# Kernel tuning notes

Measured on AMD Instinct MI355X. Metric: run time of the kernel, lower is better.

## Reference

```python
import jax, jax.numpy as jnp
import numpy as np

HEADS, DIM_HEAD, LANDMARKS, PINV_ITERS, CONV_K = 8, 64, 256, 6, 33


def iter_pinv(x, iters=PINV_ITERS):
    # Moore-Penrose iterative pseudo-inverse (lucidrains nystrom_attention)
    abs_x = jnp.abs(x)
    scale = abs_x.sum(-1).max() * abs_x.sum(-2).max()  # global maxes, as in torch.max
    z = jnp.swapaxes(x, -1, -2) / scale
    I = jnp.eye(x.shape[-1], dtype=x.dtype)
    for _ in range(iters):
        xz = x @ z
        z = 0.25 * z @ (13.0 * I - xz @ (15.0 * I - xz @ (7.0 * I - xz)))
    return z


def nystrom_attention(h, W_qkv, W_out, b_out, conv_w):
    b, n, _ = h.shape
    inner = HEADS * DIM_HEAD
    qkv = h @ W_qkv  # (b, n, 3*inner), bias=False
    q, k, v = jnp.split(qkv, 3, axis=-1)
    split_heads = lambda t: t.reshape(b, n, HEADS, DIM_HEAD).transpose(0, 2, 1, 3)
    q, k, v = split_heads(q), split_heads(k), split_heads(v)  # (b,h,n,dh)
    q = q * (DIM_HEAD ** -0.5)
    l = n // LANDMARKS  # tokens per landmark (n divisible by m, so no padding)
    q_l = q.reshape(b, HEADS, LANDMARKS, l, DIM_HEAD).mean(3)
    k_l = k.reshape(b, HEADS, LANDMARKS, l, DIM_HEAD).mean(3)
    sim1 = jnp.einsum('bhnd,bhmd->bhnm', q, k_l)      # (b,h,n,m)
    sim2 = jnp.einsum('bhmd,bhld->bhml', q_l, k_l)    # (b,h,m,m)
    sim3 = jnp.einsum('bhmd,bhnd->bhmn', q_l, k)      # (b,h,m,n)
    attn1 = jax.nn.softmax(sim1, -1)
    attn2 = jax.nn.softmax(sim2, -1)
    attn3 = jax.nn.softmax(sim3, -1)
    out = (attn1 @ iter_pinv(attn2)) @ (attn3 @ v)    # (b,h,n,dh)
    # residual depthwise conv along sequence dim: Conv2d(heads, heads, (33,1), groups=heads, no bias)
    res = jax.lax.conv_general_dilated(
        v, conv_w, window_strides=(1, 1),
        padding=((CONV_K // 2, CONV_K // 2), (0, 0)),
        feature_group_count=HEADS)
    out = out + res
    out = out.transpose(0, 2, 1, 3).reshape(b, n, inner)
    return out @ W_out + b_out


def setup_inputs() -> dict:
    key = jax.random.key(0)
    ks = jax.random.split(key, 8)
    N, Din, Dout = 8192, 1024, 256
    inner = HEADS * DIM_HEAD
    s = 0.02
    return {
        'x': jax.random.normal(ks[0], (1, N, Din), jnp.float32),
        'W_ft': jax.random.normal(ks[1], (Din, Dout), jnp.float32) * s,
        'b_ft': jnp.zeros((Dout,), jnp.float32),
        'W_qkv': jax.random.normal(ks[2], (Dout, 3 * inner), jnp.float32) * s,
        'W_out': jax.random.normal(ks[3], (inner, Dout), jnp.float32) * s,
        'b_out': jnp.zeros((Dout,), jnp.float32),
        'conv_w': jax.random.normal(ks[4], (HEADS, 1, CONV_K, 1), jnp.float32) * s,
        'W_score': jax.random.normal(ks[5], (Dout, 1), jnp.float32) * s,
        'b_score': jnp.zeros((1,), jnp.float32),
    }


def reference(x, W_ft, b_ft, W_qkv, W_out, b_out, conv_w, W_score, b_score):
    # feature_transform: Linear -> Dropout (identity in eval) -> ReLU
    h = jax.nn.relu(x @ W_ft + b_ft)                 # (1, N, Dout)
    af = nystrom_attention(h, W_qkv, W_out, b_out, conv_w)
    # score_layer: Linear -> Dropout -> ReLU
    scores = jax.nn.relu(af @ W_score + b_score)     # (1, N, 1)
    scores = scores[0].T                             # (1, N)
    weights = jax.nn.softmax(scores, axis=1)         # (1, N)
    aggregated = weights @ h[0]                      # (1, Dout)
    return aggregated, weights
```

## Files before the change

### kernel.cpp

```cpp
#include <hip/hip_runtime.h>

typedef unsigned short u16;
typedef __attribute__((ext_vector_type(8))) short s16x8;
typedef __attribute__((ext_vector_type(4))) float f32x4;
typedef __attribute__((ext_vector_type(8))) unsigned short u16x8;

__device__ inline float b2f(u16 u) {
  unsigned x = ((unsigned)u) << 16;
  return __builtin_bit_cast(float, x);
}
__device__ inline u16 f2b(float f) {
  unsigned u = __builtin_bit_cast(unsigned, f);
  u += 0x7fffu + ((u >> 16) & 1u);
  return (u16)(u >> 16);
}

#define GLL(src, dst) __builtin_amdgcn_global_load_lds( \
    (const __attribute__((address_space(1))) unsigned int*)(src), \
    (__attribute__((address_space(3))) unsigned int*)(dst), 16, 0, 0)

struct MP {
  const u16* A; const u16* B;
  u16* C; u16* Ct; float* Cf; u16* vTo;
  const u16* Aadd; const float* bias;
  int M, N, K;
  int lda, ldb, ldc, ldct, ldcf, ldaadd;
  long long bA, bB, bC, bCt, bCf, bAadd;
  float alpha, beta;
  int relu, scale_cols; float colscale;
  int kchunks;
};

template<int BM, int BN, bool F32A>
__global__ __launch_bounds__(256) void gemm_mfma(MP p)
{
  constexpr int WM = BM / 2, WN = BN / 2;
  constexpr int FM = WM / 16, FN = WN / 16;
  constexpr int APAN = BM / 16, BPAN = BN / 16, NPAN = APAN + BPAN;
  constexpr int APW = (APAN + 3) / 4;
  __shared__ __align__(16) u16 lds[2 * NPAN * 512];

  const int tid = threadIdx.x, lane = tid & 63, wid = tid >> 6;
  const int bz = blockIdx.z;
  const int batch = (p.kchunks > 1) ? bz / p.kchunks : bz;
  const int kc    = (p.kchunks > 1) ? bz % p.kchunks : 0;
  const u16* A = p.A + (long long)batch * p.bA + (long long)kc * p.K;
  const float* Af32 = (const float*)p.A + (long long)batch * p.bA + (long long)kc * p.K;
  const u16* B = p.B + (long long)batch * p.bB + (long long)kc * p.K;
  const int m0 = blockIdx.y * BM, n0 = blockIdx.x * BN;
  const int srow = lane & 15, skoff = (lane >> 4) * 8;
  const int wm0 = (wid >> 1) * WM, wn0 = (wid & 1) * WN;

  f32x4 acc[FM][FN];
#pragma unroll
  for (int i = 0; i < FM; i++)
#pragma unroll
    for (int j = 0; j < FN; j++) acc[i][j] = (f32x4){0.f, 0.f, 0.f, 0.f};

  float4 areg[APW][2];

  auto stage_all = [&](int sb, int kt) {
#pragma unroll
    for (int pp = wid; pp < NPAN; pp += 4) {
      const u16* src = (pp < APAN)
        ? A + (size_t)(m0 + pp * 16 + srow) * p.lda + kt + skoff
        : B + (size_t)(n0 + (pp - APAN) * 16 + srow) * p.ldb + kt + skoff;
      GLL(src, &lds[sb * (NPAN * 512) + pp * 512]);
    }
  };
  auto stage_b = [&](int sb, int kt) {
#pragma unroll
    for (int pp = APAN + wid; pp < NPAN; pp += 4) {
      const u16* src = B + (size_t)(n0 + (pp - APAN) * 16 + srow) * p.ldb + kt + skoff;
      GLL(src, &lds[sb * (NPAN * 512) + pp * 512]);
    }
  };
  auto load_a = [&](int kt) {
#pragma unroll
    for (int ap = 0; ap < APW; ap++) {
      int pp = wid + ap * 4;
      const float* src = Af32 + (size_t)(m0 + pp * 16 + srow) * p.lda + kt + skoff;
      areg[ap][0] = ((const float4*)src)[0];
      areg[ap][1] = ((const float4*)src)[1];
    }
  };
  auto write_a = [&](int sb) {
#pragma unroll
    for (int ap = 0; ap < APW; ap++) {
      int pp = wid + ap * 4;
      u16 t[8];
      t[0] = f2b(areg[ap][0].x); t[1] = f2b(areg[ap][0].y);
      t[2] = f2b(areg[ap][0].z); t[3] = f2b(areg[ap][0].w);
      t[4] = f2b(areg[ap][1].x); t[5] = f2b(areg[ap][1].y);
      t[6] = f2b(areg[ap][1].z); t[7] = f2b(areg[ap][1].w);
      *(s16x8*)&lds[sb * (NPAN * 512) + pp * 512 + lane * 8] = *(const s16x8*)t;
    }
  };
  auto compute = [&](int sb) {
    const int bo = sb * (NPAN * 512);
    s16x8 afr[FM], bfr[FN];
#pragma unroll
    for (int i = 0; i < FM; i++)
      afr[i] = *(const s16x8*)&lds[bo + (wm0 / 16 + i) * 512 + lane * 8];
#pragma unroll
    for (int j = 0; j < FN; j++)
      bfr[j] = *(const s16x8*)&lds[bo + (APAN + wn0 / 16 + j) * 512 + lane * 8];
#pragma unroll
    for (int i = 0; i < FM; i++)
#pragma unroll
      for (int j = 0; j < FN; j++)
        acc[i][j] = __builtin_amdgcn_mfma_f32_16x16x32_bf16(afr[i], bfr[j], acc[i][j], 0, 0, 0);
  };

  const int nt = p.K / 32;
  int buf = 0;
  if constexpr (F32A) { load_a(0); stage_b(0, 0); write_a(0); }
  else                { stage_all(0, 0); }
  asm volatile("s_waitcnt vmcnt(0)" ::: "memory");
  __syncthreads();

  for (int t = 0; t < nt; ++t) {
    if constexpr (F32A) {
      if (t + 1 < nt) { load_a((t + 1) * 32); stage_b(buf ^ 1, (t + 1) * 32); }
      compute(buf);
      if (t + 1 < nt) write_a(buf ^ 1);
    } else {
      if (t + 1 < nt) stage_all(buf ^ 1, (t + 1) * 32);
      compute(buf);
    }
    asm volatile("s_waitcnt vmcnt(0)" ::: "memory");
    __syncthreads();
    buf ^= 1;
  }

  const int r0 = (lane >> 4) * 4, c0 = lane & 15;
#pragma unroll
  for (int i = 0; i < FM; i++) {
#pragma unroll
    for (int j = 0; j < FN; j++) {
#pragma unroll
      for (int q = 0; q < 4; q++) {
        const int gr = m0 + wm0 + i * 16 + r0 + q;
        const int gc = n0 + wn0 + j * 16 + c0;
        float c = p.alpha * acc[i][j][q];
        if (p.Aadd) c += p.beta * b2f(p.Aadd[(long long)batch * p.bAadd + (size_t)gr * p.ldaadd + gc]);
        if (p.bias) c += p.bias[gc];
        if (gc < p.scale_cols) c *= p.colscale;
        if (p.relu) c = fmaxf(c, 0.f);
        if (p.Cf) p.Cf[(long long)bz * p.bCf + (size_t)gr * p.ldcf + gc] = c;
        u16 b = f2b(c);
        if (p.C)  p.C [(long long)batch * p.bC + (size_t)gr * p.ldc + gc] = b;
        if (p.Ct) p.Ct[(long long)batch * p.bCt + (size_t)gc * p.ldct + gr] = b;
        if (p.vTo && gc >= 1024) p.vTo[(size_t)(gc - 1024) * 8192 + gr] = b;
      }
    }
  }
}

struct AVF { const u16 *qkvb, *ql, *vT; float *Cf, *den; };

__global__ __launch_bounds__(256) void av_fused(AVF p)
{
  __shared__ __align__(16) u16 lds[20480];
  const int tid = threadIdx.x, lane = tid & 63, wid = tid >> 6;
  const int bz = blockIdx.z, head = bz >> 4, kc = bz & 15;
  const int m0 = blockIdx.y * 128;
  const int srow = lane & 15, skoff = (lane >> 4) * 8;
  const int r0 = (lane >> 4) * 4, c0 = lane & 15;
  const u16* Kb = p.qkvb + 512 + (size_t)(kc * 512) * 1536 + head * 64;
  const u16* Vb = p.vT + (size_t)head * 524288 + kc * 512;
  const u16* QL = p.ql + head * 16384 + (size_t)m0 * 64;

#pragma unroll
  for (int q = 0; q < 4; q++) {
    int pid = wid * 4 + q, pr = pid >> 1, kc2 = pid & 1;
    GLL(QL + (size_t)(pr * 16 + srow) * 64 + kc2 * 32 + skoff, &lds[pid * 512]);
  }
  auto stage_kv = [&](int sb, int t) {
    int kr = wid >> 1, kc2 = wid & 1;
    GLL(Kb + (size_t)(t * 32 + kr * 16 + srow) * 1536 + kc2 * 32 + skoff,
        &lds[8192 + sb * 2048 + wid * 512]);
    GLL(Vb + (size_t)(wid * 16 + srow) * 8192 + t * 32 + skoff,
        &lds[12288 + sb * 2048 + wid * 512]);
  };

  f32x4 acc[4][2];
#pragma unroll
  for (int i = 0; i < 4; i++)
#pragma unroll
    for (int j = 0; j < 2; j++) acc[i][j] = (f32x4){0.f, 0.f, 0.f, 0.f};
  float den[2][4];
#pragma unroll
  for (int i = 0; i < 2; i++)
#pragma unroll
    for (int q = 0; q < 4; q++) den[i][q] = 0.f;

  const int nt = 16;
  int buf = 0;
  stage_kv(0, 0);
  asm volatile("s_waitcnt vmcnt(0)" ::: "memory");
  __syncthreads();

  for (int t = 0; t < nt; ++t) {
    if (t + 1 < nt) stage_kv(buf ^ 1, t + 1);
    f32x4 s[2][2];
#pragma unroll
    for (int i = 0; i < 2; i++)
#pragma unroll
      for (int j = 0; j < 2; j++) s[i][j] = (f32x4){0.f, 0.f, 0.f, 0.f};
#pragma unroll
    for (int t2 = 0; t2 < 2; t2++) {
      s16x8 aq[2], bk[2];
#pragma unroll
      for (int i = 0; i < 2; i++)
        aq[i] = *(const s16x8*)&lds[((wid * 2 + i) * 2 + t2) * 512 + lane * 8];
#pragma unroll
      for (int j = 0; j < 2; j++)
        bk[j] = *(const s16x8*)&lds[8192 + buf * 2048 + (j * 2 + t2) * 512 + lane * 8];
#pragma unroll
      for (int i = 0; i < 2; i++)
#pragma unroll
        for (int j = 0; j < 2; j++)
          s[i][j] = __builtin_amdgcn_mfma_f32_16x16x32_bf16(aq[i], bk[j], s[i][j], 0, 0, 0);
    }
#pragma unroll
    for (int i = 0; i < 2; i++)
#pragma unroll
      for (int j = 0; j < 2; j++)
#pragma unroll
        for (int q = 0; q < 4; q++) {
          float e = expf(s[i][j][q]);
          den[i][q] += e;
          int kk = j * 16 + c0;
          lds[16384 + (wid * 2 + i) * 512 + (r0 + q) * 8 + (kk >> 3) * 128 + (kk & 7)] = f2b(e);
        }
    asm volatile("s_waitcnt vmcnt(0)" ::: "memory");
    __syncthreads();
    {
      s16x8 afr[4], bfr[2];
#pragma unroll
      for (int i = 0; i < 4; i++)
        afr[i] = *(const s16x8*)&lds[16384 + ((wid >> 1) * 4 + i) * 512 + lane * 8];
#pragma unroll
      for (int j = 0; j < 2; j++)
        bfr[j] = *(const s16x8*)&lds[12288 + buf * 2048 + ((wid & 1) * 2 + j) * 512 + lane * 8];
#pragma unroll
      for (int i = 0; i < 4; i++)
#pragma unroll
        for (int j = 0; j < 2; j++)
          acc[i][j] = __builtin_amdgcn_mfma_f32_16x16x32_bf16(afr[i], bfr[j], acc[i][j], 0, 0, 0);
    }
    __syncthreads();
    buf ^= 1;
  }

#pragma unroll
  for (int i = 0; i < 4; i++)
#pragma unroll
    for (int j = 0; j < 2; j++)
#pragma unroll
      for (int q = 0; q < 4; q++) {
        const int gr = m0 + (wid >> 1) * 64 + i * 16 + r0 + q;
        const int gc = (wid & 1) * 32 + j * 16 + c0;
        p.Cf[(size_t)bz * 16384 + (size_t)gr * 64 + gc] = acc[i][j][q];
      }
#pragma unroll
  for (int i = 0; i < 2; i++)
#pragma unroll
    for (int q = 0; q < 4; q++) {
      float v = den[i][q];
      v += __shfl_xor(v, 1); v += __shfl_xor(v, 2);
      v += __shfl_xor(v, 4); v += __shfl_xor(v, 8);
      if (c0 == 0)
        p.den[(size_t)bz * 256 + m0 + wid * 32 + i * 16 + r0 + q] = v;
    }
}

struct FA1 { const u16 *qkvb, *kl, *MmT; u16 *af; };

__global__ __launch_bounds__(256) void fused_attn1(FA1 p)
{
  __shared__ __align__(16) u16 lds[36864];
  __shared__ float mb[4][64];
  const int tid = threadIdx.x, lane = tid & 63, wid = tid >> 6;
  const int head = blockIdx.y, n0 = blockIdx.x * 64;
  const int srow = lane & 15, skoff = (lane >> 4) * 8;
  const int rbase = (lane >> 4) * 4;

  for (int pid = wid; pid < 72; pid += 4) {
    const u16* src;
    if (pid < 8) {
      int pr = pid >> 1, kc = pid & 1;
      src = p.qkvb + (size_t)(n0 + pr * 16 + srow) * 1536 + head * 64 + kc * 32 + skoff;
    } else if (pid < 40) {
      int j = pid - 8, pr = j >> 1, kc = j & 1;
      src = p.kl + head * 16384 + (size_t)(pr * 16 + srow) * 64 + kc * 32 + skoff;
    } else {
      int j = pid - 40, pr = j >> 3, kc = j & 7;
      src = p.MmT + head * 16384 + (size_t)(pr * 16 + srow) * 256 + kc * 32 + skoff;
    }
    GLL(src, &lds[pid * 512]);
  }
  asm volatile("s_waitcnt vmcnt(0)" ::: "memory");
  __syncthreads();

  const int wr = (wid >> 1) * 32, ch_ = wid & 1;
  f32x4 s[2][8];
#pragma unroll
  for (int i = 0; i < 2; i++)
#pragma unroll
    for (int j = 0; j < 8; j++) s[i][j] = (f32x4){0.f, 0.f, 0.f, 0.f};
#pragma unroll
  for (int t = 0; t < 2; t++) {
    s16x8 a[2], b[8];
#pragma unroll
    for (int i = 0; i < 2; i++)
      a[i] = *(const s16x8*)&lds[(((wid >> 1) * 2 + i) * 2 + t) * 512 + lane * 8];
#pragma unroll
    for (int j = 0; j < 8; j++)
      b[j] = *(const s16x8*)&lds[4096 + ((ch_ * 8 + j) * 2 + t) * 512 + lane * 8];
#pragma unroll
    for (int i = 0; i < 2; i++)
#pragma unroll
      for (int j = 0; j < 8; j++)
        s[i][j] = __builtin_amdgcn_mfma_f32_16x16x32_bf16(a[i], b[j], s[i][j], 0, 0, 0);
  }
#pragma unroll
  for (int i = 0; i < 2; i++)
#pragma unroll
    for (int q = 0; q < 4; q++) {
      float rm = -INFINITY;
#pragma unroll
      for (int j = 0; j < 8; j++) rm = fmaxf(rm, s[i][j][q]);
#pragma unroll
      for (int off = 1; off < 16; off <<= 1) rm = fmaxf(rm, __shfl_xor(rm, off));
      if ((lane & 15) == 0) mb[ch_][wr + i * 16 + rbase + q] = rm;
    }
  __syncthreads();
  float m_[2][4];
#pragma unroll
  for (int i = 0; i < 2; i++)
#pragma unroll
    for (int q = 0; q < 4; q++)
      m_[i][q] = fmaxf(mb[0][wr + i * 16 + rbase + q], mb[1][wr + i * 16 + rbase + q]);
#pragma unroll
  for (int i = 0; i < 2; i++)
#pragma unroll
    for (int q = 0; q < 4; q++) {
      float ss = 0.f;
#pragma unroll
      for (int j = 0; j < 8; j++) {
        float e = expf(s[i][j][q] - m_[i][q]);
        s[i][j][q] = e; ss += e;
      }
#pragma unroll
      for (int off = 1; off < 16; off <<= 1) ss += __shfl_xor(ss, off);
      if ((lane & 15) == 0) mb[2 + ch_][wr + i * 16 + rbase + q] = ss;
    }
  __syncthreads();
#pragma unroll
  for (int i = 0; i < 2; i++)
#pragma unroll
    for (int q = 0; q < 4; q++) {
      int row = wr + i * 16 + rbase + q;
      float inv = 1.f / (mb[2][row] + mb[3][row]);
#pragma unroll
      for (int j = 0; j < 8; j++)
        lds[(size_t)row * 264 + ch_ * 128 + j * 16 + (lane & 15)] = f2b(s[i][j][q] * inv);
    }
  __syncthreads();
  const int wr2 = (wid >> 1) * 32, wd2 = (wid & 1) * 32;
  f32x4 acc[2][2];
#pragma unroll
  for (int i = 0; i < 2; i++)
#pragma unroll
    for (int jd = 0; jd < 2; jd++) acc[i][jd] = (f32x4){0.f, 0.f, 0.f, 0.f};
#pragma unroll
  for (int t = 0; t < 8; t++) {
    s16x8 a[2], b[2];
#pragma unroll
    for (int i = 0; i < 2; i++)
      a[i] = *(const s16x8*)&lds[(size_t)(wr2 + i * 16 + (lane & 15)) * 264 + t * 32 + (lane >> 4) * 8];
#pragma unroll
    for (int jd = 0; jd < 2; jd++)
      b[jd] = *(const s16x8*)&lds[20480 + (((wid & 1) * 2 + jd) * 8 + t) * 512 + lane * 8];
#pragma unroll
    for (int i = 0; i < 2; i++)
#pragma unroll
      for (int jd = 0; jd < 2; jd++)
        acc[i][jd] = __builtin_amdgcn_mfma_f32_16x16x32_bf16(a[i], b[jd], acc[i][jd], 0, 0, 0);
  }
#pragma unroll
  for (int i = 0; i < 2; i++)
#pragma unroll
    for (int jd = 0; jd < 2; jd++)
#pragma unroll
      for (int q = 0; q < 4; q++)
        p.af[(size_t)(n0 + wr2 + i * 16 + rbase + q) * 512 + head * 64 + wd2 + jd * 16 + (lane & 15)]
            = f2b(acc[i][jd][q]);
}

__global__ void conv_res_add_bf16(const u16* __restrict__ qkvb,
                                  const float* __restrict__ convw,
                                  u16* __restrict__ af)
{
  __shared__ float vt[96][64];
  const int h = blockIdx.y, n0 = blockIdx.x * 64;
  const int t = threadIdx.x, ch = t & 63, r0 = t >> 6;
  for (int r = r0; r < 96; r += 4) {
    int n = n0 - 16 + r;
    float v = 0.f;
    if (n >= 0 && n < 8192) v = b2f(qkvb[(size_t)n * 1536 + 1024 + h * 64 + ch]);
    vt[r][ch] = v;
  }
  __syncthreads();
  float w[33];
#pragma unroll
  for (int j = 0; j < 33; j++) w[j] = convw[h * 33 + j];
  for (int tl = r0; tl < 64; tl += 4) {
    float acc = 0.f;
#pragma unroll
    for (int j = 0; j < 33; j++) acc += w[j] * vt[tl + j][ch];
    size_t o = (size_t)(n0 + tl) * 512 + h * 64 + ch;
    af[o] = f2b(b2f(af[o]) + acc);
  }
}

__global__ void reduce_bias_bf16(const float* __restrict__ parts, int nparts,
                                 const float* __restrict__ bias, int relu,
                                 u16* __restrict__ out,
                                 const float* __restrict__ Wscore,
                                 const float* __restrict__ bscore,
                                 float* __restrict__ scores)
{
  const int i4 = blockIdx.x * 256 + threadIdx.x;
  float4 s = ((const float4*)parts)[i4];
  for (int k = 1; k < nparts; k++) {
    float4 v = ((const float4*)parts)[(size_t)k * 524288 + i4];
    s.x += v.x; s.y += v.y; s.z += v.z; s.w += v.w;
  }
  const float4 b = ((const float4*)bias)[i4 & 63];
  s.x += b.x; s.y += b.y; s.z += b.z; s.w += b.w;
  if (relu) {
    s.x = fmaxf(s.x, 0.f); s.y = fmaxf(s.y, 0.f);
    s.z = fmaxf(s.z, 0.f); s.w = fmaxf(s.w, 0.f);
  }
  if (out) {
    ushort4 o; o.x = f2b(s.x); o.y = f2b(s.y); o.z = f2b(s.z); o.w = f2b(s.w);
    ((ushort4*)out)[i4] = o;
  }
  if (Wscore) {
    const int lane = threadIdx.x & 63;
    const float4 w = ((const float4*)Wscore)[lane];
    float v = s.x * w.x + s.y * w.y + s.z * w.z + s.w * w.w;
    for (int off = 32; off; off >>= 1) v += __shfl_down(v, off);
    if (lane == 0)
      scores[blockIdx.x * 4 + (threadIdx.x >> 6)] = fmaxf(v + bscore[0], 0.f);
  }
}

__global__ void fused_tail(const float* __restrict__ scores,
                           const u16* __restrict__ hb, float* __restrict__ out)
{
  __shared__ float red[256];
  const int t = threadIdx.x, c = blockIdx.x;
  float e[32];
  float m = -INFINITY;
#pragma unroll
  for (int i = 0; i < 32; i++) { e[i] = scores[t + i * 256]; m = fmaxf(m, e[i]); }
  red[t] = m; __syncthreads();
  for (int s = 128; s; s >>= 1) { if (t < s) red[t] = fmaxf(red[t], red[t + s]); __syncthreads(); }
  m = red[0]; __syncthreads();
  float ls = 0.f;
#pragma unroll
  for (int i = 0; i < 32; i++) { e[i] = expf(e[i] - m); ls += e[i]; }
  red[t] = ls; __syncthreads();
  for (int s = 128; s; s >>= 1) { if (t < s) red[t] += red[t + s]; __syncthreads(); }
  const float inv = 1.f / red[0];
  __syncthreads();

  if (c < 256) {
    float acc = 0.f;
#pragma unroll
    for (int i = 0; i < 32; i++)
      acc += e[i] * inv * b2f(hb[(size_t)(t + i * 256) * 256 + c]);
    red[t] = acc; __syncthreads();
    for (int s = 128; s; s >>= 1) { if (t < s) red[t] += red[t + s]; __syncthreads(); }
    if (t == 0) out[c] = red[0];
  } else {
#pragma unroll
    for (int i = 0; i < 32; i++) out[256 + t + i * 256] = e[i] * inv;
  }
}

__global__ void prescale(const u16* __restrict__ x2, float* __restrict__ sbuf)
{
  const int h = blockIdx.x, t = threadIdx.x;
  const u16* X = x2 + ((size_t)h << 16);
  float cs = 0.f;
  for (int r = 0; r < 256; r++) cs += fabsf(b2f(X[r * 256 + t]));
  float rs = 0.f;
  for (int c4 = 0; c4 < 256; c4 += 4) {
    ushort4 v = *(const ushort4*)(X + (size_t)t * 256 + c4);
    rs += fabsf(b2f(v.x)) + fabsf(b2f(v.y)) + fabsf(b2f(v.z)) + fabsf(b2f(v.w));
  }
  __shared__ float red[512];
  red[t] = rs; red[256 + t] = cs;
  __syncthreads();
  for (int s = 128; s; s >>= 1) {
    if (t < s) {
      red[t] = fmaxf(red[t], red[t + s]);
      red[256 + t] = fmaxf(red[256 + t], red[256 + t + s]);
    }
    __syncthreads();
  }
  if (t == 0) { sbuf[h] = red[0]; sbuf[8 + h] = red[256]; }
}

__global__ void pinv_init(const u16* __restrict__ x2, const float* __restrict__ sbuf,
                          u16* __restrict__ z0, u16* __restrict__ z0T)
{
  __shared__ u16 tile[64][80];
  const int t = threadIdx.x;
  const size_t base = (size_t)blockIdx.y << 16;
  const int tr = (blockIdx.x >> 2) * 64, tc = (blockIdx.x & 3) * 64;
  const u16* X = x2 + base;

  float mr = -INFINITY, mc = -INFINITY;
#pragma unroll
  for (int i = 0; i < 8; i++) {
    mr = fmaxf(mr, sbuf[i]);
    mc = fmaxf(mc, sbuf[8 + i]);
  }
  const float inv = 1.f / (mr * mc);

  {
    int r = t >> 2, cg = (t & 3) * 16;
#pragma unroll
    for (int v4 = 0; v4 < 4; v4++) {
      ushort4 v = *(const ushort4*)(X + (size_t)(tr + r) * 256 + tc + cg + v4 * 4);
      v.x = f2b(b2f(v.x) * inv); v.y = f2b(b2f(v.y) * inv);
      v.z = f2b(b2f(v.z) * inv); v.w = f2b(b2f(v.w) * inv);
      *(ushort4*)(z0T + base + (size_t)(tr + r) * 256 + tc + cg + v4 * 4) = v;
      *(ushort4*)&tile[r][cg + v4 * 4] = v;
    }
  }
  __syncthreads();
  {
    int c = t >> 2, rg = (t & 3) * 16;
    u16 o[16];
#pragma unroll
    for (int e = 0; e < 16; e++) o[e] = tile[rg + e][c];
#pragma unroll
    for (int v4 = 0; v4 < 4; v4++)
      *(ushort4*)(z0 + base + (size_t)(tc + c) * 256 + tr + rg + v4 * 4) = *(ushort4*)&o[v4 * 4];
  }
}

struct PG {
  const u16 *U, *V, *Xadd, *XaddT;
  u16 *DR, *DT;
  float alpha, beta;
};

template<bool WD, bool WDT>
__global__ __launch_bounds__(256) void pinv_gemm(PG p)
{
  __shared__ __align__(16) u16 lds[65536 / 2];
  const int tid = threadIdx.x, lane = tid & 63, wid = tid >> 6;
  const size_t base = (size_t)blockIdx.z << 16;
  const u16* U = p.U + base;
  const u16* V = p.V + base;
  const int m0 = blockIdx.y * 64, n0 = blockIdx.x * 64;
  const int srow = lane & 15, skoff = (lane >> 4) * 8;
  const int wr = (wid >> 1) * 32, wc = (wid & 1) * 32;

#pragma unroll
  for (int q = 0; q < 16; q++) {
    const int pid = wid * 16 + q;
    const int rg = (pid >> 3) & 3, t = pid & 7;
    const u16* src = (pid < 32)
      ? U + (size_t)(m0 + rg * 16 + srow) * 256 + t * 32 + skoff
      : V + (size_t)(n0 + rg * 16 + srow) * 256 + t * 32 + skoff;
    GLL(src, &lds[pid * 512]);
  }
  asm volatile("s_waitcnt vmcnt(0)" ::: "memory");
  __syncthreads();

  f32x4 acc[2][2], accT[2][2];
#pragma unroll
  for (int i = 0; i < 2; i++)
#pragma unroll
    for (int j = 0; j < 2; j++) {
      acc[i][j] = (f32x4){0.f, 0.f, 0.f, 0.f};
      accT[i][j] = (f32x4){0.f, 0.f, 0.f, 0.f};
    }

#pragma unroll
  for (int t = 0; t < 8; t++) {
    s16x8 afr[2], bfr[2];
#pragma unroll
    for (int i = 0; i < 2; i++)
      afr[i] = *(const s16x8*)&lds[((wr / 16 + i) * 8 + t) * 512 + lane * 8];
#pragma unroll
    for (int j = 0; j < 2; j++)
      bfr[j] = *(const s16x8*)&lds[(32 + (wc / 16 + j) * 8 + t) * 512 + lane * 8];
#pragma unroll
    for (int i = 0; i < 2; i++)
#pragma unroll
      for (int j = 0; j < 2; j++) {
        if constexpr (WD)
          acc[i][j] = __builtin_amdgcn_mfma_f32_16x16x32_bf16(afr[i], bfr[j], acc[i][j], 0, 0, 0);
        if constexpr (WDT)
          accT[j][i] = __builtin_amdgcn_mfma_f32_16x16x32_bf16(bfr[j], afr[i], accT[j][i], 0, 0, 0);
      }
  }

  const int r0 = (lane >> 4) * 4, c0 = lane & 15;
  if constexpr (WD) {
    const u16* Xa = p.Xadd ? p.Xadd + base : nullptr;
    u16* DR = p.DR + base;
#pragma unroll
    for (int i = 0; i < 2; i++)
#pragma unroll
      for (int j = 0; j < 2; j++)
#pragma unroll
        for (int q = 0; q < 4; q++) {
          const int gr = m0 + wr + i * 16 + r0 + q;
          const int gc = n0 + wc + j * 16 + c0;
          float v = p.alpha * acc[i][j][q];
          if (Xa) v += p.beta * b2f(Xa[(size_t)gr * 256 + gc]);
          DR[(size_t)gr * 256 + gc] = f2b(v);
        }
  }
  if constexpr (WDT) {
    const u16* Xt = p.XaddT ? p.XaddT + base : nullptr;
    u16* DT = p.DT + base;
#pragma unroll
    for (int j = 0; j < 2; j++)
#pragma unroll
      for (int i = 0; i < 2; i++)
#pragma unroll
        for (int q = 0; q < 4; q++) {
          const int gn = n0 + wc + j * 16 + r0 + q;
          const int gm = m0 + wr + i * 16 + c0;
          float v = p.alpha * accT[j][i][q];
          if (Xt) v += p.beta * b2f(Xt[(size_t)gn * 256 + gm]);
          DT[(size_t)gn * 256 + gm] = f2b(v);
        }
  }
}

struct PR1 { const u16 *A, *At, *z; u16 *B, *Bt, *G, *Gt, *W; };

__global__ __launch_bounds__(256) void pinv_r1(PR1 p)
{
  __shared__ __align__(16) u16 lds[32768];
  const int tid = threadIdx.x, lane = tid & 63, wid = tid >> 6;
  const int prob = blockIdx.z >> 3;
  const size_t base = (size_t)(blockIdx.z & 7) << 16;
  const u16* U = (prob ? p.z : p.A) + base;
  const u16* V = p.At + base;
  const int m0 = blockIdx.y * 64, n0 = blockIdx.x * 64;
  const int srow = lane & 15, skoff = (lane >> 4) * 8;
  const int wr = (wid >> 1) * 32, wc = (wid & 1) * 32;

#pragma unroll
  for (int q = 0; q < 16; q++) {
    const int pid = wid * 16 + q;
    const int rg = (pid >> 3) & 3, t = pid & 7;
    const u16* src = (pid < 32)
      ? U + (size_t)(m0 + rg * 16 + srow) * 256 + t * 32 + skoff
      : V + (size_t)(n0 + rg * 16 + srow) * 256 + t * 32 + skoff;
    GLL(src, &lds[pid * 512]);
  }
  asm volatile("s_waitcnt vmcnt(0)" ::: "memory");
  __syncthreads();

  f32x4 acc[2][2], accT[2][2];
#pragma unroll
  for (int i = 0; i < 2; i++)
#pragma unroll
    for (int j = 0; j < 2; j++) {
      acc[i][j] = (f32x4){0.f, 0.f, 0.f, 0.f};
      accT[i][j] = (f32x4){0.f, 0.f, 0.f, 0.f};
    }

#pragma unroll
  for (int t = 0; t < 8; t++) {
    s16x8 afr[2], bfr[2];
#pragma unroll
    for (int i = 0; i < 2; i++)
      afr[i] = *(const s16x8*)&lds[((wr / 16 + i) * 8 + t) * 512 + lane * 8];
#pragma unroll
    for (int j = 0; j < 2; j++)
      bfr[j] = *(const s16x8*)&lds[(32 + (wc / 16 + j) * 8 + t) * 512 + lane * 8];
#pragma unroll
    for (int i = 0; i < 2; i++)
#pragma unroll
      for (int j = 0; j < 2; j++) {
        acc[i][j] = __builtin_amdgcn_mfma_f32_16x16x32_bf16(afr[i], bfr[j], acc[i][j], 0, 0, 0);
        if (prob == 0)
          accT[j][i] = __builtin_amdgcn_mfma_f32_16x16x32_bf16(bfr[j], afr[i], accT[j][i], 0, 0, 0);
      }
  }

  const int r0 = (lane >> 4) * 4, c0 = lane & 15;
  if (prob == 0) {
    const u16* Ab  = p.A  + base;
    const u16* Atb = p.At + base;
    u16 *Bv = p.B + base, *Btv = p.Bt + base;
    u16 *Gv = p.G + base, *Gtv = p.Gt + base;
#pragma unroll
    for (int i = 0; i < 2; i++)
#pragma unroll
      for (int j = 0; j < 2; j++)
#pragma unroll
        for (int q = 0; q < 4; q++) {
          const int gr = m0 + wr + i * 16 + r0 + q;
          const int gc = n0 + wc + j * 16 + c0;
          float b = acc[i][j][q];
          float a = b2f(Ab[(size_t)gr * 256 + gc]);
          Bv[(size_t)gr * 256 + gc] = f2b(b);
          Gv[(size_t)gr * 256 + gc] = f2b(7.f * a - b);
        }
#pragma unroll
    for (int j = 0; j < 2; j++)
#pragma unroll
      for (int i = 0; i < 2; i++)
#pragma unroll
        for (int q = 0; q < 4; q++) {
          const int gn = n0 + wc + j * 16 + r0 + q;
          const int gm = m0 + wr + i * 16 + c0;
          float bt = accT[j][i][q];
          float at = b2f(Atb[(size_t)gn * 256 + gm]);
          Btv[(size_t)gn * 256 + gm] = f2b(bt);
          Gtv[(size_t)gn * 256 + gm] = f2b(7.f * at - bt);
        }
  } else {
    u16* Wv = p.W + base;
#pragma unroll
    for (int i = 0; i < 2; i++)
#pragma unroll
      for (int j = 0; j < 2; j++)
#pragma unroll
        for (int q = 0; q < 4; q++) {
          const int gr = m0 + wr + i * 16 + r0 + q;
          const int gc = n0 + wc + j * 16 + c0;
          Wv[(size_t)gr * 256 + gc] = f2b(acc[i][j][q]);
        }
  }
}

struct PR2 { const u16 *W, *G, *Gt, *B, *Bt, *z, *A, *At; u16 *zo, *Ao, *Aot; };

__global__ __launch_bounds__(256) void pinv_r2(PR2 p)
{
  __shared__ __align__(16) u16 lds[32768];
  const int tid = threadIdx.x, lane = tid & 63, wid = tid >> 6;
  const int prob = blockIdx.z >> 3;
  const size_t base = (size_t)(blockIdx.z & 7) << 16;
  const u16* U = (prob ? p.G  : p.W ) + base;
  const u16* V = (prob ? p.Bt : p.Gt) + base;
  const int m0 = blockIdx.y * 64, n0 = blockIdx.x * 64;
  const int srow = lane & 15, skoff = (lane >> 4) * 8;
  const int wr = (wid >> 1) * 32, wc = (wid & 1) * 32;

#pragma unroll
  for (int q = 0; q < 16; q++) {
    const int pid = wid * 16 + q;
    const int rg = (pid >> 3) & 3, t = pid & 7;
    const u16* src = (pid < 32)
      ? U + (size_t)(m0 + rg * 16 + srow) * 256 + t * 32 + skoff
      : V + (size_t)(n0 + rg * 16 + srow) * 256 + t * 32 + skoff;
    GLL(src, &lds[pid * 512]);
  }
  asm volatile("s_waitcnt vmcnt(0)" ::: "memory");
  __syncthreads();

  f32x4 acc[2][2], accT[2][2];
#pragma unroll
  for (int i = 0; i < 2; i++)
#pragma unroll
    for (int j = 0; j < 2; j++) {
      acc[i][j] = (f32x4){0.f, 0.f, 0.f, 0.f};
      accT[i][j] = (f32x4){0.f, 0.f, 0.f, 0.f};
    }

#pragma unroll
  for (int t = 0; t < 8; t++) {
    s16x8 afr[2], bfr[2];
#pragma unroll
    for (int i = 0; i < 2; i++)
      afr[i] = *(const s16x8*)&lds[((wr / 16 + i) * 8 + t) * 512 + lane * 8];
#pragma unroll
    for (int j = 0; j < 2; j++)
      bfr[j] = *(const s16x8*)&lds[(32 + (wc / 16 + j) * 8 + t) * 512 + lane * 8];
#pragma unroll
    for (int i = 0; i < 2; i++)
#pragma unroll
      for (int j = 0; j < 2; j++) {
        acc[i][j] = __builtin_amdgcn_mfma_f32_16x16x32_bf16(afr[i], bfr[j], acc[i][j], 0, 0, 0);
        if (prob)
          accT[j][i] = __builtin_amdgcn_mfma_f32_16x16x32_bf16(bfr[j], afr[i], accT[j][i], 0, 0, 0);
      }
  }

  const int r0 = (lane >> 4) * 4, c0 = lane & 15;
  if (prob == 0) {
    const u16* Zb = p.z + base;
    const u16* Wb = p.W + base;
    u16* Zo = p.zo + base;
#pragma unroll
    for (int i = 0; i < 2; i++)
#pragma unroll
      for (int j = 0; j < 2; j++)
#pragma unroll
        for (int q = 0; q < 4; q++) {
          const int gr = m0 + wr + i * 16 + r0 + q;
          const int gc = n0 + wc + j * 16 + c0;
          float v = 0.25f * acc[i][j][q]
                  + 3.25f * b2f(Zb[(size_t)gr * 256 + gc])
                  - 3.75f * b2f(Wb[(size_t)gr * 256 + gc]);
          Zo[(size_t)gr * 256 + gc] = f2b(v);
        }
  } else {
    const u16* Ab  = p.A  + base;
    const u16* Bb  = p.B  + base;
    const u16* Atb = p.At + base;
    const u16* Btb = p.Bt + base;
    u16* Ao  = p.Ao  + base;
    u16* Aot = p.Aot + base;
#pragma unroll
    for (int i = 0; i < 2; i++)
#pragma unroll
      for (int j = 0; j < 2; j++)
#pragma unroll
        for (int q = 0; q < 4; q++) {
          const int gr = m0 + wr + i * 16 + r0 + q;
          const int gc = n0 + wc + j * 16 + c0;
          float v = 0.25f * acc[i][j][q]
                  + 3.25f * b2f(Ab[(size_t)gr * 256 + gc])
                  - 3.75f * b2f(Bb[(size_t)gr * 256 + gc]);
          Ao[(size_t)gr * 256 + gc] = f2b(v);
        }
#pragma unroll
    for (int j = 0; j < 2; j++)
#pragma unroll
      for (int i = 0; i < 2; i++)
#pragma unroll
        for (int q = 0; q < 4; q++) {
          const int gn = n0 + wc + j * 16 + r0 + q;
          const int gm = m0 + wr + i * 16 + c0;
          float v = 0.25f * accT[j][i][q]
                  + 3.25f * b2f(Atb[(size_t)gn * 256 + gm])
                  - 3.75f * b2f(Btb[(size_t)gn * 256 + gm]);
          Aot[(size_t)gn * 256 + gm] = f2b(v);
        }
  }
}

__global__ void prep_weights(const float* __restrict__ Wft, const float* __restrict__ Wqkv,
                             const float* __restrict__ Wout, u16* __restrict__ WftT,
                             u16* __restrict__ WqkvT, u16* __restrict__ WoutT)
{
  int idx = blockIdx.x * 256 + threadIdx.x;
  if (idx < 262144) {
    int r = idx & 1023, c = idx >> 10;
    WftT[idx] = f2b(Wft[(size_t)r * 256 + c]);
  } else if (idx < 655360) {
    int i = idx - 262144;
    int r = i & 255, c = i >> 8;
    WqkvT[i] = f2b(Wqkv[(size_t)r * 1536 + c]);
  } else {
    int i = idx - 655360;
    int r = i & 511, c = i >> 9;
    WoutT[i] = f2b(Wout[(size_t)r * 256 + c]);
  }
}

__global__ void landmark_means(const u16* __restrict__ qkvb,
                               u16* __restrict__ ql, u16* __restrict__ kl)
{
  int idx = blockIdx.x * 256 + threadIdx.x;
  int which = idx >> 17, r = idx & 131071;
  int h = r >> 14, m = (r >> 6) & 255, d = r & 63;
  const u16* src = qkvb + (which ? 512 : 0) + h * 64 + d;
  float s = 0.f; int n0 = m * 32;
  for (int i = 0; i < 32; i++) s += b2f(src[(size_t)(n0 + i) * 1536]);
  (which ? kl : ql)[r] = f2b(s * (1.f / 32.f));
}

__global__ void softmax_rows_bf16_256(u16* __restrict__ d)
{
  const int row = blockIdx.x * 4 + (threadIdx.x >> 6);
  const int lane = threadIdx.x & 63;
  ushort4* p = (ushort4*)(d + (size_t)row * 256);
  ushort4 raw = p[lane];
  float v0 = b2f(raw.x), v1 = b2f(raw.y), v2 = b2f(raw.z), v3 = b2f(raw.w);
  float mx = fmaxf(fmaxf(v0, v1), fmaxf(v2, v3));
  for (int off = 1; off < 64; off <<= 1) mx = fmaxf(mx, __shfl_xor(mx, off));
  v0 = expf(v0 - mx); v1 = expf(v1 - mx); v2 = expf(v2 - mx); v3 = expf(v3 - mx);
  float s = v0 + v1 + v2 + v3;
  for (int off = 1; off < 64; off <<= 1) s += __shfl_xor(s, off);
  float inv = 1.f / s;
  raw.x = f2b(v0 * inv); raw.y = f2b(v1 * inv); raw.z = f2b(v2 * inv); raw.w = f2b(v3 * inv);
  p[lane] = raw;
}

__global__ void reduce_avT(const float* __restrict__ avp, const float* __restrict__ den,
                           u16* __restrict__ avT)
{
  int idx = blockIdx.x * 256 + threadIdx.x;
  int m = idx & 255, d = (idx >> 8) & 63, h = idx >> 14;
  float s = 0.f, l = 0.f;
  for (int c = 0; c < 16; c++) {
    s += avp[((size_t)(h * 16 + c)) * 16384 + m * 64 + d];
    l += den[(size_t)(h * 16 + c) * 256 + m];
  }
  avT[((size_t)h * 64 + d) * 256 + m] = f2b(s / l);
}

extern "C" void kernel_launch(void* const* d_in, const int* in_sizes, int n_in,
                              void* d_out, int out_size, void* d_ws, size_t ws_size,
                              hipStream_t stream)
{
  const float* x       = (const float*)d_in[0];
  const float* W_ft    = (const float*)d_in[1];
  const float* b_ft    = (const float*)d_in[2];
  const float* W_qkv   = (const float*)d_in[3];
  const float* W_out   = (const float*)d_in[4];
  const float* b_out   = (const float*)d_in[5];
  const float* conv_w  = (const float*)d_in[6];
  const float* W_score = (const float*)d_in[7];
  const float* b_score = (const float*)d_in[8];
  float* out = (float*)d_out;

  char* W = (char*)d_ws;
  auto alloc = [&](size_t bytes) { char* r = W; W += (bytes + 255) & ~(size_t)255; return r; };
  u16* WftT  = (u16*)alloc(256ull * 1024 * 2);
  u16* WqkvT = (u16*)alloc(1536ull * 256 * 2);
  u16* WoutT = (u16*)alloc(256ull * 512 * 2);
  u16* hb    = (u16*)alloc(8192ull * 256 * 2);
  u16* qkvb  = (u16*)alloc(8192ull * 1536 * 2);
  u16* ql    = (u16*)alloc(8ull * 256 * 64 * 2);
  u16* kl    = (u16*)alloc(8ull * 256 * 64 * 2);
  u16* x2    = (u16*)alloc(8ull * 256 * 256 * 2);
  u16* z0    = (u16*)alloc(8ull * 256 * 256 * 2);
  u16* z0T   = (u16*)alloc(8ull * 256 * 256 * 2);
  u16* zp    = (u16*)alloc(8ull * 256 * 256 * 2);
  u16* Amat  = (u16*)alloc(8ull * 256 * 256 * 2);
  u16* AmatT = (u16*)alloc(8ull * 256 * 256 * 2);
  u16* Am2   = (u16*)alloc(8ull * 256 * 256 * 2);
  u16* Am2T  = (u16*)alloc(8ull * 256 * 256 * 2);
  u16* Bm    = (u16*)alloc(8ull * 256 * 256 * 2);
  u16* BmT   = (u16*)alloc(8ull * 256 * 256 * 2);
  u16* Gm    = (u16*)alloc(8ull * 256 * 256 * 2);
  u16* GmT   = (u16*)alloc(8ull * 256 * 256 * 2);
  u16* Wm    = (u16*)alloc(8ull * 256 * 256 * 2);
  u16* vT    = (u16*)alloc(8ull * 64 * 8192 * 2);
  float* avp = (float*)alloc(8ull * 16 * 256 * 64 * 4);
  float* denp = (float*)alloc(128ull * 256 * 4);
  u16* avT   = (u16*)alloc(8ull * 64 * 256 * 2);
  u16* MmT   = (u16*)alloc(8ull * 64 * 256 * 2);
  u16* af    = (u16*)alloc(8192ull * 512 * 2);
  float* gpart = (float*)alloc(4ull * 8192 * 256 * 4);
  float* sbuf   = (float*)alloc(256);
  float* scores = (float*)alloc(8192 * 4);

  auto mp = [](const u16* A, const u16* B, int M, int N, int K,
               int lda, int ldb, long long bA, long long bB) {
    MP p{}; p.A = A; p.B = B; p.M = M; p.N = N; p.K = K;
    p.lda = lda; p.ldb = ldb; p.bA = bA; p.bB = bB;
    p.alpha = 1.f; p.beta = 0.f; p.kchunks = 1; return p;
  };

  prep_weights<<<3072, 256, 0, stream>>>(W_ft, W_qkv, W_out, WftT, WqkvT, WoutT);

  { MP p = mp((const u16*)x, WftT, 8192, 256, 256, 1024, 1024, 0, 0);
    p.kchunks = 4; p.Cf = gpart; p.ldcf = 256; p.bCf = 2097152;
    gemm_mfma<64, 256, true><<<dim3(1, 128, 4), 256, 0, stream>>>(p); }
  reduce_bias_bf16<<<2048, 256, 0, stream>>>(gpart, 4, b_ft, 1, hb,
                                             nullptr, nullptr, nullptr);

  { MP p = mp(hb, WqkvT, 8192, 1536, 256, 256, 256, 0, 0);
    p.C = qkvb; p.ldc = 1536; p.scale_cols = 512; p.colscale = 0.125f; p.vTo = vT;
    gemm_mfma<128, 128, false><<<dim3(12, 64, 1), 256, 0, stream>>>(p); }

  landmark_means<<<1024, 256, 0, stream>>>(qkvb, ql, kl);

  { MP p = mp(ql, kl, 256, 256, 64, 64, 64, 16384, 16384);
    p.C = x2; p.ldc = 256; p.bC = 65536;
    gemm_mfma<64, 64, false><<<dim3(4, 4, 8), 256, 0, stream>>>(p); }
  softmax_rows_bf16_256<<<512, 256, 0, stream>>>(x2);

  prescale<<<8, 256, 0, stream>>>(x2, sbuf);
  pinv_init<<<dim3(16, 8), 256, 0, stream>>>(x2, sbuf, z0, z0T);
  { PG p{x2, z0T, nullptr, nullptr, Amat, AmatT, 1.f, 0.f};
    pinv_gemm<true, true><<<dim3(4, 4, 8), 256, 0, stream>>>(p); }
  {
    const dim3 b(256);
    u16 *zr = z0, *zo = zp;
    u16 *Ar = Amat, *Art = AmatT, *Ao = Am2, *Aot = Am2T;
    for (int it = 0; it < 6; it++) {
      { PR1 r{Ar, Art, zr, Bm, BmT, Gm, GmT, Wm};
        pinv_r1<<<dim3(4, 4, 16), b, 0, stream>>>(r); }
      { PR2 r{Wm, Gm, GmT, Bm, BmT, zr, Ar, Art, zo, Ao, Aot};
        pinv_r2<<<dim3(4, 4, (it == 5) ? 8 : 16), b, 0, stream>>>(r); }
      u16* t;
      t = zr; zr = zo; zo = t;
      t = Ar; Ar = Ao; Ao = t;
      t = Art; Art = Aot; Aot = t;
    }
  }

  { AVF p{qkvb, ql, vT, avp, denp};
    av_fused<<<dim3(1, 2, 128), 256, 0, stream>>>(p); }
  reduce_avT<<<512, 256, 0, stream>>>(avp, denp, avT);

  { MP p = mp(z0, avT, 256, 64, 256, 256, 256, 65536, 16384);
    p.Ct = MmT; p.ldct = 256; p.bCt = 16384;
    gemm_mfma<64, 64, false><<<dim3(1, 4, 8), 256, 0, stream>>>(p); }

  { FA1 fp{qkvb, kl, MmT, af};
    fused_attn1<<<dim3(128, 8), 256, 0, stream>>>(fp); }

  conv_res_add_bf16<<<dim3(128, 8), 256, 0, stream>>>(qkvb, conv_w, af);

  { MP p = mp(af, WoutT, 8192, 256, 128, 512, 512, 0, 0);
    p.kchunks = 4; p.Cf = gpart; p.ldcf = 256; p.bCf = 2097152;
    gemm_mfma<64, 256, false><<<dim3(1, 128, 4), 256, 0, stream>>>(p); }
  reduce_bias_bf16<<<2048, 256, 0, stream>>>(gpart, 4, b_out, 0, nullptr,
                                             W_score, b_score, scores);

  fused_tail<<<257, 256, 0, stream>>>(scores, hb, out);
}
```

Baseline: 343.8 us.

## Drop split-K partial buffers; fuse bias, ReLU and score projection into GEMM epilogues

Result: slower. 357.9 us (+4.1%).

```diff
diff --git a/kernel.cpp b/kernel.cpp
--- a/kernel.cpp
+++ b/kernel.cpp
@@ -23,6 +23,7 @@
   const u16* A; const u16* B;
   u16* C; u16* Ct; float* Cf; u16* vTo;
   const u16* Aadd; const float* bias;
+  const float* Ws; float* sc; const float* wconst;
   int M, N, K;
   int lda, ldb, ldc, ldct, ldcf, ldaadd;
   long long bA, bB, bC, bCt, bCf, bAadd;
@@ -134,6 +135,29 @@
   }
 
   const int r0 = (lane >> 4) * 4, c0 = lane & 15;
+
+  if (p.Ws) {
+    float* sb = (float*)lds;
+#pragma unroll
+    for (int i = 0; i < FM; i++)
+#pragma unroll
+      for (int q = 0; q < 4; q++) {
+        float s = 0.f;
+#pragma unroll
+        for (int j = 0; j < FN; j++)
+          s += acc[i][j][q] * p.Ws[wn0 + j * 16 + c0];
+        s += __shfl_xor(s, 1); s += __shfl_xor(s, 2);
+        s += __shfl_xor(s, 4); s += __shfl_xor(s, 8);
+        if ((lane & 15) == 0) sb[(wid & 1) * 64 + wm0 + i * 16 + r0 + q] = s;
+      }
+    __syncthreads();
+    if (tid < 64) {
+      float v = sb[tid] + sb[64 + tid] + p.wconst[0];
+      p.sc[m0 + tid] = fmaxf(v, 0.f);
+    }
+    return;
+  }
+
 #pragma unroll
   for (int i = 0; i < FM; i++) {
 #pragma unroll
@@ -423,39 +447,6 @@
     for (int j = 0; j < 33; j++) acc += w[j] * vt[tl + j][ch];
     size_t o = (size_t)(n0 + tl) * 512 + h * 64 + ch;
     af[o] = f2b(b2f(af[o]) + acc);
-  }
-}
-
-__global__ void reduce_bias_bf16(const float* __restrict__ parts, int nparts,
-                                 const float* __restrict__ bias, int relu,
-                                 u16* __restrict__ out,
-                                 const float* __restrict__ Wscore,
-                                 const float* __restrict__ bscore,
-                                 float* __restrict__ scores)
-{
-  const int i4 = blockIdx.x * 256 + threadIdx.x;
-  float4 s = ((const float4*)parts)[i4];
-  for (int k = 1; k < nparts; k++) {
-    float4 v = ((const float4*)parts)[(size_t)k * 524288 + i4];
-    s.x += v.x; s.y += v.y; s.z += v.z; s.w += v.w;
-  }
-  const float4 b = ((const float4*)bias)[i4 & 63];
-  s.x += b.x; s.y += b.y; s.z += b.z; s.w += b.w;
-  if (relu) {
-    s.x = fmaxf(s.x, 0.f); s.y = fmaxf(s.y, 0.f);
-    s.z = fmaxf(s.z, 0.f); s.w = fmaxf(s.w, 0.f);
-  }
-  if (out) {
-    ushort4 o; o.x = f2b(s.x); o.y = f2b(s.y); o.z = f2b(s.z); o.w = f2b(s.w);
-    ((ushort4*)out)[i4] = o;
-  }
-  if (Wscore) {
-    const int lane = threadIdx.x & 63;
-    const float4 w = ((const float4*)Wscore)[lane];
-    float v = s.x * w.x + s.y * w.y + s.z * w.z + s.w * w.w;
-    for (int off = 32; off; off >>= 1) v += __shfl_down(v, off);
-    if (lane == 0)
-      scores[blockIdx.x * 4 + (threadIdx.x >> 6)] = fmaxf(v + bscore[0], 0.f);
   }
 }
 
@@ -862,9 +853,18 @@
 
 __global__ void prep_weights(const float* __restrict__ Wft, const float* __restrict__ Wqkv,
                              const float* __restrict__ Wout, u16* __restrict__ WftT,
-                             u16* __restrict__ WqkvT, u16* __restrict__ WoutT)
+                             u16* __restrict__ WqkvT, u16* __restrict__ WoutT,
+                             const float* __restrict__ bout, const float* __restrict__ Wsc,
+                             const float* __restrict__ bsc, float* __restrict__ wconst)
 {
   int idx = blockIdx.x * 256 + threadIdx.x;
+  if (blockIdx.x == 0 && threadIdx.x < 64) {
+    int c = threadIdx.x * 4;
+    float s = bout[c] * Wsc[c] + bout[c + 1] * Wsc[c + 1]
+            + bout[c + 2] * Wsc[c + 2] + bout[c + 3] * Wsc[c + 3];
+    for (int off = 1; off < 64; off <<= 1) s += __shfl_xor(s, off);
+    if (threadIdx.x == 0) wconst[0] = s + bsc[0];
+  }
   if (idx < 262144) {
     int r = idx & 1023, c = idx >> 10;
     WftT[idx] = f2b(Wft[(size_t)r * 256 + c]);
@@ -964,9 +964,9 @@
   u16* avT   = (u16*)alloc(8ull * 64 * 256 * 2);
   u16* MmT   = (u16*)alloc(8ull * 64 * 256 * 2);
   u16* af    = (u16*)alloc(8192ull * 512 * 2);
-  float* gpart = (float*)alloc(4ull * 8192 * 256 * 4);
   float* sbuf   = (float*)alloc(256);
   float* scores = (float*)alloc(8192 * 4);
+  float* wconst = (float*)alloc(256);
 
   auto mp = [](const u16* A, const u16* B, int M, int N, int K,
                int lda, int ldb, long long bA, long long bB) {
@@ -975,13 +975,12 @@
     p.alpha = 1.f; p.beta = 0.f; p.kchunks = 1; return p;
   };
 
-  prep_weights<<<3072, 256, 0, stream>>>(W_ft, W_qkv, W_out, WftT, WqkvT, WoutT);
-
-  { MP p = mp((const u16*)x, WftT, 8192, 256, 256, 1024, 1024, 0, 0);
-    p.kchunks = 4; p.Cf = gpart; p.ldcf = 256; p.bCf = 2097152;
-    gemm_mfma<64, 256, true><<<dim3(1, 128, 4), 256, 0, stream>>>(p); }
-  reduce_bias_bf16<<<2048, 256, 0, stream>>>(gpart, 4, b_ft, 1, hb,
-                                             nullptr, nullptr, nullptr);
+  prep_weights<<<3072, 256, 0, stream>>>(W_ft, W_qkv, W_out, WftT, WqkvT, WoutT,
+                                         b_out, W_score, b_score, wconst);
+
+  { MP p = mp((const u16*)x, WftT, 8192, 256, 1024, 1024, 1024, 0, 0);
+    p.C = hb; p.ldc = 256; p.bias = b_ft; p.relu = 1;
+    gemm_mfma<64, 256, true><<<dim3(1, 128, 1), 256, 0, stream>>>(p); }
 
   { MP p = mp(hb, WqkvT, 8192, 1536, 256, 256, 256, 0, 0);
     p.C = qkvb; p.ldc = 1536; p.scale_cols = 512; p.colscale = 0.125f; p.vTo = vT;
@@ -1027,11 +1026,9 @@
 
   conv_res_add_bf16<<<dim3(128, 8), 256, 0, stream>>>(qkvb, conv_w, af);
 
-  { MP p = mp(af, WoutT, 8192, 256, 128, 512, 512, 0, 0);
-    p.kchunks = 4; p.Cf = gpart; p.ldcf = 256; p.bCf = 2097152;
-    gemm_mfma<64, 256, false><<<dim3(1, 128, 4), 256, 0, stream>>>(p); }
-  reduce_bias_bf16<<<2048, 256, 0, stream>>>(gpart, 4, b_out, 0, nullptr,
-                                             W_score, b_score, scores);
+  { MP p = mp(af, WoutT, 8192, 256, 512, 512, 512, 0, 0);
+    p.Ws = W_score; p.sc = scores; p.wconst = wconst;
+    gemm_mfma<64, 256, false><<<dim3(1, 128, 1), 256, 0, stream>>>(p); }
 
   fused_tail<<<257, 256, 0, stream>>>(scores, hb, out);
 }
```
